# Kernel tuning notes

Measured on AMD Instinct MI355X. Metric: run time of the kernel, lower is better.

Reference implementation:

```python
import jax, jax.numpy as jnp
import numpy as np

T, D, E, F = 8192, 1024, 8, 3584


def setup_inputs() -> dict:
    key = jax.random.key(0)
    ks = jax.random.split(key, 5)
    scale_in = 1.0 / np.sqrt(D)
    scale_ff = 1.0 / np.sqrt(F)
    return {
        "x": jax.random.normal(ks[0], (T, D), dtype=jnp.float32),
        "w1": jax.random.normal(ks[1], (E, F, D), dtype=jnp.float32) * scale_in,
        "w3": jax.random.normal(ks[2], (E, F, D), dtype=jnp.float32) * scale_in,
        "w2": jax.random.normal(ks[3], (E, D, F), dtype=jnp.float32) * scale_ff,
        "router_logits": jax.random.normal(ks[4], (T, E), dtype=jnp.float32),
        "top_k": 2,
    }


def reference(x, w1, w3, w2, router_logits, top_k):
    # Routing: softmax over experts, keep top-k, renormalize (Mixtral, normalize=True)
    probs = jax.nn.softmax(router_logits, axis=-1)            # [T, E]
    top_vals, top_idx = jax.lax.top_k(probs, top_k)           # [T, k]
    top_vals = top_vals / jnp.sum(top_vals, axis=-1, keepdims=True)
    tokens = jnp.arange(x.shape[0])[:, None]
    weights = jnp.zeros_like(probs).at[tokens, top_idx].set(top_vals)  # [T, E]

    gate = jnp.einsum('td,efd->tef', x, w1)                   # [T, E, F]
    up = jnp.einsum('td,efd->tef', x, w3)                     # [T, E, F]
    h = jax.nn.silu(gate) * up                                # [T, E, F]
    out = jnp.einsum('te,tef,edf->td', weights, h, w2)        # [T, D]
    return out
```

## Files before the change

kernel.cpp:

```cpp
#include <hip/hip_runtime.h>
#include <cstdint>

#define T_TOK 8192
#define D_DIM 1024
#define E_EXP 8
#define F_DIM 3584
#define NROW  (2 * T_TOK)
#define PROWS_PAD 18432

typedef __attribute__((ext_vector_type(8))) __bf16 bf16x8;
typedef __attribute__((ext_vector_type(4))) float f32x4;

__device__ __forceinline__ void gload16(const void* g, void* l) {
    __builtin_amdgcn_global_load_lds(
        (const __attribute__((address_space(1))) void*)(g),
        (__attribute__((address_space(3))) void*)(l),
        16, 0, 0);
}

__device__ __forceinline__ int xcd_swz(int bid, int nwg) {
    const int nx = 8;
    const int q = nwg / nx, r = nwg % nx;
    const int xcd = bid % nx, lid = bid / nx;
    return (xcd < r ? xcd * (q + 1) : r * (q + 1) + (xcd - r) * q) + lid;
}

__global__ void cvt_kernel(const float* __restrict__ in, __bf16* __restrict__ out, long n) {
    long i = ((long)blockIdx.x * blockDim.x + threadIdx.x) * 8;
    if (i >= n) return;
    const float4 f0 = *(const float4*)(in + i);
    const float4 f1 = *(const float4*)(in + i + 4);
    bf16x8 o;
    o[0] = (__bf16)f0.x; o[1] = (__bf16)f0.y; o[2] = (__bf16)f0.z; o[3] = (__bf16)f0.w;
    o[4] = (__bf16)f1.x; o[5] = (__bf16)f1.y; o[6] = (__bf16)f1.z; o[7] = (__bf16)f1.w;
    *(bf16x8*)(out + i) = o;
}

__global__ void route_kernel(const float* __restrict__ rl, int* cnt,
                             int* __restrict__ eidx, float* __restrict__ ewgt) {
    int t = blockIdx.x * blockDim.x + threadIdx.x;
    if (t >= T_TOK) return;
    float l[8];
#pragma unroll
    for (int e = 0; e < 8; ++e) l[e] = rl[t * 8 + e];
    int i0 = 0; float v0 = l[0];
    int i1 = -1; float v1 = -1e30f;
#pragma unroll
    for (int e = 1; e < 8; ++e) {
        if (l[e] > v0) { v1 = v0; i1 = i0; v0 = l[e]; i0 = e; }
        else if (l[e] > v1) { v1 = l[e]; i1 = e; }
    }
    float wsec = 1.f / (1.f + __expf(v0 - v1));
    eidx[2 * t] = i0; eidx[2 * t + 1] = i1;
    ewgt[2 * t] = 1.f - wsec; ewgt[2 * t + 1] = wsec;
    atomicAdd(&cnt[i0], 1); atomicAdd(&cnt[i1], 1);
}

__global__ void scan_kernel(const int* __restrict__ cnt, int* __restrict__ pofs) {
    if (threadIdx.x == 0) {
        int a = 0;
        for (int e = 0; e < E_EXP; ++e) { pofs[e] = a; a += (cnt[e] + 255) & ~255; }
        pofs[E_EXP] = a;
    }
}

__global__ void assign_kernel(const int* __restrict__ eidx, const int* __restrict__ pofs,
                              int* cnt2, int* __restrict__ tokOf, int* __restrict__ rowOf) {
    int t = blockIdx.x * blockDim.x + threadIdx.x;
    if (t >= T_TOK) return;
#pragma unroll
    for (int s = 0; s < 2; ++s) {
        int e = eidx[2 * t + s];
        int pos = atomicAdd(&cnt2[e], 1);
        int prow = pofs[e] + pos;
        tokOf[prow] = t;
        rowOf[2 * t + s] = prow;
    }
}

__global__ void gather_kernel(const float* __restrict__ x, const int* __restrict__ tokOf,
                              __bf16* __restrict__ xg) {
    const int idx = blockIdx.x * blockDim.x + threadIdx.x;
    const int pr = idx >> 7;
    const int j = (idx & 127) * 8;
    const int tk = tokOf[pr];
    bf16x8 o = {};
    if (tk >= 0) {
        const float4 f0 = *(const float4*)(x + (long)tk * D_DIM + j);
        const float4 f1 = *(const float4*)(x + (long)tk * D_DIM + j + 4);
        o[0] = (__bf16)f0.x; o[1] = (__bf16)f0.y; o[2] = (__bf16)f0.z; o[3] = (__bf16)f0.w;
        o[4] = (__bf16)f1.x; o[5] = (__bf16)f1.y; o[6] = (__bf16)f1.z; o[7] = (__bf16)f1.w;
    }
    *(bf16x8*)(xg + (long)pr * D_DIM + j) = o;
}

__device__ __forceinline__ int chunk_row(int c) { return ((c >> 7) << 4) | ((c >> 2) & 15); }
__device__ __forceinline__ int chunk_col(int c) {
    return ((c >> 6) & 1) * 32 + (((c & 3) * 8) ^ (((c >> 5) & 1) << 4));
}

template <int NT>
__device__ __forceinline__ void moe_pipeline(
    const __bf16* const (&srcA)[2][2], const __bf16* const (&srcB)[2][2],
    __bf16 (&Ash)[2][2][8192], __bf16 (&Bsh)[2][2][8192],
    int wave, int abase, int wm, int bh, int bsel, f32x4 (&acc)[8][4])
{
    auto stA = [&](int buf, int kt, int h) {
        const long k0 = (long)kt * 64;
        gload16(srcA[h][0] + k0, &Ash[buf][h][(0 * 512 + wave * 64) * 8]);
        gload16(srcA[h][1] + k0, &Ash[buf][h][(1 * 512 + wave * 64) * 8]);
    };
    auto stB = [&](int buf, int kt, int h) {
        const long k0 = (long)kt * 64;
        gload16(srcB[h][0] + k0, &Bsh[buf][h][(0 * 512 + wave * 64) * 8]);
        gload16(srcB[h][1] + k0, &Bsh[buf][h][(1 * 512 + wave * 64) * 8]);
    };

    bf16x8 bfr[4][2];
    bf16x8 a0, a1, a2, a3;

#define LD_A(Ab, q) \
    a0 = *(const bf16x8*)((Ab) + ((2*(q)) * 2 + 0) * 512); \
    a1 = *(const bf16x8*)((Ab) + ((2*(q)) * 2 + 1) * 512); \
    a2 = *(const bf16x8*)((Ab) + ((2*(q)+1) * 2 + 0) * 512); \
    a3 = *(const bf16x8*)((Ab) + ((2*(q)+1) * 2 + 1) * 512);

#define LD_B(Bb) \
    _Pragma("unroll") for (int ni = 0; ni < 4; ++ni) { \
        bfr[ni][0] = *(const bf16x8*)((Bb) + ((bsel * 4 + ni) * 2 + 0) * 512); \
        bfr[ni][1] = *(const bf16x8*)((Bb) + ((bsel * 4 + ni) * 2 + 1) * 512); \
    }

#define MFMA_Q(q) \
    _Pragma("unroll") for (int ni = 0; ni < 4; ++ni) { \
        acc[2*(q)][ni]   = __builtin_amdgcn_mfma_f32_16x16x32_bf16(a0, bfr[ni][0], acc[2*(q)][ni], 0, 0, 0); \
        acc[2*(q)][ni]   = __builtin_amdgcn_mfma_f32_16x16x32_bf16(a1, bfr[ni][1], acc[2*(q)][ni], 0, 0, 0); \
        acc[2*(q)+1][ni] = __builtin_amdgcn_mfma_f32_16x16x32_bf16(a2, bfr[ni][0], acc[2*(q)+1][ni], 0, 0, 0); \
        acc[2*(q)+1][ni] = __builtin_amdgcn_mfma_f32_16x16x32_bf16(a3, bfr[ni][1], acc[2*(q)+1][ni], 0, 0, 0); \
    }

#define PH_OPEN() \
    __builtin_amdgcn_sched_barrier(0); \
    __builtin_amdgcn_s_barrier(); \
    asm volatile("s_waitcnt lgkmcnt(0)" ::: "memory"); \
    __builtin_amdgcn_sched_barrier(0); \
    __builtin_amdgcn_s_setprio(1);

#define PH_CLOSE() \
    __builtin_amdgcn_s_setprio(0); \
    __builtin_amdgcn_sched_barrier(0); \
    __builtin_amdgcn_s_barrier(); \
    __builtin_amdgcn_sched_barrier(0);

#define PH_CLOSE_G(lastf) \
    __builtin_amdgcn_s_setprio(0); \
    __builtin_amdgcn_sched_barrier(0); \
    if (lastf) { asm volatile("s_waitcnt vmcnt(0)" ::: "memory"); } \
    else       { asm volatile("s_waitcnt vmcnt(4)" ::: "memory"); } \
    __builtin_amdgcn_s_barrier(); \
    __builtin_amdgcn_sched_barrier(0);

    stA(0, 0, 0); stA(0, 0, 1); stB(0, 0, 0); stB(0, 0, 1);
    stB(1, 1, 0); stB(1, 1, 1);
    asm volatile("s_waitcnt vmcnt(4)" ::: "memory");
    __builtin_amdgcn_s_barrier();

    const __bf16* AbE = &Ash[0][wm][abase];
    const __bf16* BbE = &Bsh[0][bh][abase];
    const __bf16* AbO = &Ash[1][wm][abase];
    const __bf16* BbO = &Bsh[1][bh][abase];

    for (int it = 0; it < NT / 2; ++it) {
        const int kv = 2 * it + 1;
        const bool last = (it == NT / 2 - 1);
        LD_A(AbE, 0) LD_B(BbE)
        stA(1, kv, 0);
        PH_OPEN() MFMA_Q(0) PH_CLOSE()
        LD_A(AbE, 1)
        stA(1, kv, 1);
        PH_OPEN() MFMA_Q(1) PH_CLOSE()
        LD_A(AbE, 2)
        if (!last) stB(0, kv + 1, 0);
        PH_OPEN() MFMA_Q(2) PH_CLOSE()
        LD_A(AbE, 3)
        if (!last) stB(0, kv + 1, 1);
        PH_OPEN() MFMA_Q(3) PH_CLOSE_G(last)
        LD_A(AbO, 0) LD_B(BbO)
        if (!last) stA(0, kv + 1, 0);
        PH_OPEN() MFMA_Q(0) PH_CLOSE()
        LD_A(AbO, 1)
        if (!last) stA(0, kv + 1, 1);
        PH_OPEN() MFMA_Q(1) PH_CLOSE()
        LD_A(AbO, 2)
        if (!last) stB(1, kv + 2, 0);
        PH_OPEN() MFMA_Q(2) PH_CLOSE()
        LD_A(AbO, 3)
        if (!last) stB(1, kv + 2, 1);
        PH_OPEN() MFMA_Q(3) PH_CLOSE_G(last)
    }
#undef LD_A
#undef LD_B
#undef MFMA_Q
#undef PH_OPEN
#undef PH_CLOSE
#undef PH_CLOSE_G
}

__global__ __launch_bounds__(512, 1)
void gemm1_kernel(const __bf16* __restrict__ xg,
                  const __bf16* __restrict__ w1b,
                  const __bf16* __restrict__ w3b,
                  const int* __restrict__ pofs,
                  __bf16* __restrict__ h) {
    const int NX = F_DIM / 128, NY = T_TOK / 256;
    const int nwg = NX * NY * E_EXP;
    int w = xcd_swz(blockIdx.x + NX * (blockIdx.y + NY * blockIdx.z), nwg);
    const int nt = w % NX; w /= NX;
    const int mt = w % NY; w /= NY;
    const int e = w;
    const int row0 = pofs[e];
    const int prows = pofs[e + 1] - row0;
    if (mt * 256 >= prows) return;

    __shared__ __align__(16) __bf16 Ash[2][2][8192];
    __shared__ __align__(16) __bf16 Bsh[2][2][8192];

    const int tid = threadIdx.x;
    const int wave = tid >> 6, lane = tid & 63;
    const int wm = wave >> 2, wn = wave & 3;
    const int fr = lane & 15, fg = lane >> 4;

    const __bf16* srcA[2][2];
    const __bf16* srcB[2][2];
#pragma unroll
    for (int half = 0; half < 2; ++half)
#pragma unroll
        for (int j = 0; j < 2; ++j) {
            const int c = tid + j * 512;
            srcA[half][j] = xg + (long)(row0 + mt * 256 + half * 128 + chunk_row(c)) * D_DIM + chunk_col(c);
            const int rb = half * 128 + chunk_row(c);
            const int blk = rb >> 4;
            const int f = nt * 128 + (blk >> 1) * 16 + (rb & 15);
            srcB[half][j] = ((blk & 1) ? w3b : w1b) + ((long)e * F_DIM + f) * D_DIM + chunk_col(c);
        }

    const int abase = fr * 32 + ((fg * 8) ^ ((fr & 8) << 1));
    f32x4 acc[8][4] = {};

    moe_pipeline<16>(srcA, srcB, Ash, Bsh, wave, abase, wm, wn >> 1, wn & 1, acc);

#pragma unroll
    for (int mi = 0; mi < 8; ++mi) {
#pragma unroll
        for (int reg = 0; reg < 4; ++reg) {
            const int lm = mt * 256 + wm * 128 + mi * 16 + fg * 4 + reg;
            const long hrow = (long)(row0 + lm) * F_DIM;
#pragma unroll
            for (int b = 0; b < 2; ++b) {
                const float g = acc[mi][2 * b][reg];
                const float u = acc[mi][2 * b + 1][reg];
                const float s = g / (1.f + __expf(-g));
                h[hrow + nt * 128 + (wn * 2 + b) * 16 + fr] = (__bf16)(s * u);
            }
        }
    }
}

__global__ __launch_bounds__(512, 1)
void gemm2_kernel(const __bf16* __restrict__ hb,
                  const __bf16* __restrict__ w2b,
                  const int* __restrict__ pofs,
                  __bf16* __restrict__ o2p) {
    const int NX = D_DIM / 256, NY = T_TOK / 256;
    const int nwg = NX * NY * E_EXP * 2;
    int w = xcd_swz(blockIdx.x + NX * (blockIdx.y + NY * blockIdx.z), nwg);
    const int nt = w % NX; w /= NX;
    const int mt = w % NY; w /= NY;
    const int e = w >> 1, ks = w & 1;
    const int row0 = pofs[e];
    const int prows = pofs[e + 1] - row0;
    if (mt * 256 >= prows) return;

    __shared__ __align__(16) __bf16 Ash[2][2][8192];
    __shared__ __align__(16) __bf16 Bsh[2][2][8192];

    const int tid = threadIdx.x;
    const int wave = tid >> 6, lane = tid & 63;
    const int wm = wave >> 2, wn = wave & 3;
    const int fr = lane & 15, fg = lane >> 4;
    const int kofs = ks * (F_DIM / 2);

    const __bf16* srcA[2][2];
    const __bf16* srcB[2][2];
#pragma unroll
    for (int half = 0; half < 2; ++half)
#pragma unroll
        for (int j = 0; j < 2; ++j) {
            const int c = tid + j * 512;
            srcA[half][j] = hb + (long)(row0 + mt * 256 + half * 128 + chunk_row(c)) * F_DIM + kofs + chunk_col(c);
            const int rb = half * 128 + chunk_row(c);
            srcB[half][j] = w2b + ((long)e * D_DIM + nt * 256 + rb) * F_DIM + kofs + chunk_col(c);
        }

    const int abase = fr * 32 + ((fg * 8) ^ ((fr & 8) << 1));
    f32x4 acc[8][4] = {};

    moe_pipeline<28>(srcA, srcB, Ash, Bsh, wave, abase, wm, wn >> 1, wn & 1, acc);

    __bf16* ps = o2p + (long)ks * PROWS_PAD * D_DIM;
#pragma unroll
    for (int mi = 0; mi < 8; ++mi) {
#pragma unroll
        for (int reg = 0; reg < 4; ++reg) {
            const int lm = mt * 256 + wm * 128 + mi * 16 + fg * 4 + reg;
            const long obase = (long)(row0 + lm) * D_DIM + nt * 256 + wn * 64 + fr;
#pragma unroll
            for (int ni = 0; ni < 4; ++ni)
                ps[obase + ni * 16] = (__bf16)acc[mi][ni][reg];
        }
    }
}

__global__ void combine_kernel(const __bf16* __restrict__ o2p, const int* __restrict__ rowOf,
                               const float* __restrict__ ewgt, float* __restrict__ out) {
    const int idx = blockIdx.x * blockDim.x + threadIdx.x;
    const int t = idx >> 7;
    const int j = (idx & 127) * 8;
    const long r0 = rowOf[2 * t], r1 = rowOf[2 * t + 1];
    const float w0 = ewgt[2 * t], w1 = ewgt[2 * t + 1];
    float r[8] = {0, 0, 0, 0, 0, 0, 0, 0};
#pragma unroll
    for (int s = 0; s < 2; ++s) {
        const bf16x8 a = *(const bf16x8*)(o2p + ((long)s * PROWS_PAD + r0) * D_DIM + j);
        const bf16x8 b = *(const bf16x8*)(o2p + ((long)s * PROWS_PAD + r1) * D_DIM + j);
#pragma unroll
        for (int q = 0; q < 8; ++q) r[q] += w0 * (float)a[q] + w1 * (float)b[q];
    }
    float4* ob = (float4*)(out + (long)t * D_DIM + j);
    ob[0] = make_float4(r[0], r[1], r[2], r[3]);
    ob[1] = make_float4(r[4], r[5], r[6], r[7]);
}

extern "C" void kernel_launch(void* const* d_in, const int* in_sizes, int n_in,
                              void* d_out, int out_size, void* d_ws, size_t ws_size,
                              hipStream_t stream) {
    const float* x  = (const float*)d_in[0];
    const float* w1 = (const float*)d_in[1];
    const float* w3 = (const float*)d_in[2];
    const float* w2 = (const float*)d_in[3];
    const float* rl = (const float*)d_in[4];
    float* out = (float*)d_out;

    char* ws = (char*)d_ws;
    size_t off = 0;
    auto alloc = [&](size_t bytes) {
        void* p = ws + off;
        off += (bytes + 255) & ~(size_t)255;
        return p;
    };
    __bf16* xg   = (__bf16*)alloc((size_t)PROWS_PAD * D_DIM * 2);
    __bf16* w1b  = (__bf16*)alloc((size_t)E_EXP * F_DIM * D_DIM * 2);
    __bf16* w3b  = (__bf16*)alloc((size_t)E_EXP * F_DIM * D_DIM * 2);
    __bf16* hbuf = (__bf16*)alloc((size_t)PROWS_PAD * F_DIM * 2);
    int*   tokOf = (int*)alloc(PROWS_PAD * 4);
    int*   rowOf = (int*)alloc(NROW * 4);
    int*   eidx  = (int*)alloc(NROW * 4);
    float* ewgt  = (float*)alloc(NROW * 4);
    int*   cnt1  = (int*)alloc(64);
    int*   cnt2  = (int*)alloc(64);
    int*   pofs  = (int*)alloc(64);
    __bf16* w2b = (__bf16*)ws;
    __bf16* o2p = (__bf16*)(ws + (size_t)E_EXP * D_DIM * F_DIM * 2);

    hipMemsetAsync(cnt1, 0, 64, stream);
    hipMemsetAsync(cnt2, 0, 64, stream);
    hipMemsetAsync(tokOf, 0xFF, PROWS_PAD * 4, stream);

    route_kernel<<<T_TOK / 256, 256, 0, stream>>>(rl, cnt1, eidx, ewgt);
    scan_kernel<<<1, 64, 0, stream>>>(cnt1, pofs);
    assign_kernel<<<T_TOK / 256, 256, 0, stream>>>(eidx, pofs, cnt2, tokOf, rowOf);
    gather_kernel<<<PROWS_PAD * 128 / 256, 256, 0, stream>>>(x, tokOf, xg);

    {
        const long n = (long)E_EXP * F_DIM * D_DIM;
        const int blks = (int)(n / 8 / 256);
        cvt_kernel<<<blks, 256, 0, stream>>>(w1, w1b, n);
        cvt_kernel<<<blks, 256, 0, stream>>>(w3, w3b, n);
    }

    dim3 g1(F_DIM / 128, T_TOK / 256, E_EXP);
    gemm1_kernel<<<g1, 512, 0, stream>>>(xg, w1b, w3b, pofs, hbuf);

    {
        const long n = (long)E_EXP * D_DIM * F_DIM;
        cvt_kernel<<<(int)(n / 8 / 256), 256, 0, stream>>>(w2, w2b, n);
    }

    dim3 g2(D_DIM / 256, T_TOK / 256, E_EXP * 2);
    gemm2_kernel<<<g2, 512, 0, stream>>>(hbuf, w2b, pofs, o2p);

    combine_kernel<<<T_TOK * (D_DIM / 8) / 256, 256, 0, stream>>>(o2p, rowOf, ewgt, out);
}
```

Before: 701.5 us.

## Schedule GEMM workgroups from a compact tile list with banded L2-friendly ordering

Adds a tiles kernel that lists every (expert, 256-row) tile actually in use. Both grouped GEMMs now launch a 1D grid over this compact list instead of a dense (N, M, E) grid where most blocks exit early. Tiles are grouped into bands of four, and each XCD gets a contiguous range of work so neighbouring blocks share A rows and weight columns in cache. The cost is one extra serial kernel launch and a new block-to-tile mapping that replaces the old XCD swizzle.

```diff
diff --git a/kernel.cpp b/kernel.cpp
--- a/kernel.cpp
+++ b/kernel.cpp
@@ -7,6 +7,8 @@
 #define F_DIM 3584
 #define NROW  (2 * T_TOK)
 #define PROWS_PAD 18432
+#define MAXTILES 72
+#define MAXBANDS 18
 
 typedef __attribute__((ext_vector_type(8))) __bf16 bf16x8;
 typedef __attribute__((ext_vector_type(4))) float f32x4;
@@ -16,13 +18,6 @@
         (const __attribute__((address_space(1))) void*)(g),
         (__attribute__((address_space(3))) void*)(l),
         16, 0, 0);
-}
-
-__device__ __forceinline__ int xcd_swz(int bid, int nwg) {
-    const int nx = 8;
-    const int q = nwg / nx, r = nwg % nx;
-    const int xcd = bid % nx, lid = bid / nx;
-    return (xcd < r ? xcd * (q + 1) : r * (q + 1) + (xcd - r) * q) + lid;
 }
 
 __global__ void cvt_kernel(const float* __restrict__ in, __bf16* __restrict__ out, long n) {
@@ -61,6 +56,18 @@
         int a = 0;
         for (int e = 0; e < E_EXP; ++e) { pofs[e] = a; a += (cnt[e] + 255) & ~255; }
         pofs[E_EXP] = a;
+    }
+}
+
+__global__ void tiles_kernel(const int* __restrict__ pofs, int* __restrict__ tile_e,
+                             int* __restrict__ tile_r0, int* __restrict__ meta) {
+    if (threadIdx.x == 0) {
+        int n = 0;
+        for (int e = 0; e < E_EXP; ++e)
+            for (int r = pofs[e]; r < pofs[e + 1]; r += 256) {
+                tile_e[n] = e; tile_r0[n] = r; ++n;
+            }
+        meta[0] = n;
     }
 }
 
@@ -210,17 +217,22 @@
 void gemm1_kernel(const __bf16* __restrict__ xg,
                   const __bf16* __restrict__ w1b,
                   const __bf16* __restrict__ w3b,
-                  const int* __restrict__ pofs,
+                  const int* __restrict__ tile_e,
+                  const int* __restrict__ tile_r0,
+                  const int* __restrict__ meta,
                   __bf16* __restrict__ h) {
-    const int NX = F_DIM / 128, NY = T_TOK / 256;
-    const int nwg = NX * NY * E_EXP;
-    int w = xcd_swz(blockIdx.x + NX * (blockIdx.y + NY * blockIdx.z), nwg);
-    const int nt = w % NX; w /= NX;
-    const int mt = w % NY; w /= NY;
-    const int e = w;
-    const int row0 = pofs[e];
-    const int prows = pofs[e + 1] - row0;
-    if (mt * 256 >= prows) return;
+    const int count = meta[0];
+    const int bands = (count + 3) >> 2;
+    const int live = bands * 112;
+    const int bid = blockIdx.x;
+    if (bid >= live) return;
+    const int w = (bid & 7) * (live >> 3) + (bid >> 3);
+    const int q28 = w / 28, r = w % 28;
+    const int tile = (q28 >> 2) * 4 + r / 7;
+    const int nt = (q28 & 3) * 7 + r % 7;
+    if (tile >= count) return;
+    const int e = tile_e[tile];
+    const int row0 = tile_r0[tile];
 
     __shared__ __align__(16) __bf16 Ash[2][2][8192];
     __shared__ __align__(16) __bf16 Bsh[2][2][8192];
@@ -237,7 +249,7 @@
 #pragma unroll
         for (int j = 0; j < 2; ++j) {
             const int c = tid + j * 512;
-            srcA[half][j] = xg + (long)(row0 + mt * 256 + half * 128 + chunk_row(c)) * D_DIM + chunk_col(c);
+            srcA[half][j] = xg + (long)(row0 + half * 128 + chunk_row(c)) * D_DIM + chunk_col(c);
             const int rb = half * 128 + chunk_row(c);
             const int blk = rb >> 4;
             const int f = nt * 128 + (blk >> 1) * 16 + (rb & 15);
@@ -253,7 +265,7 @@
     for (int mi = 0; mi < 8; ++mi) {
 #pragma unroll
         for (int reg = 0; reg < 4; ++reg) {
-            const int lm = mt * 256 + wm * 128 + mi * 16 + fg * 4 + reg;
+            const int lm = wm * 128 + mi * 16 + fg * 4 + reg;
             const long hrow = (long)(row0 + lm) * F_DIM;
 #pragma unroll
             for (int b = 0; b < 2; ++b) {
@@ -269,17 +281,22 @@
 __global__ __launch_bounds__(512, 1)
 void gemm2_kernel(const __bf16* __restrict__ hb,
                   const __bf16* __restrict__ w2b,
-                  const int* __restrict__ pofs,
+                  const int* __restrict__ tile_e,
+                  const int* __restrict__ tile_r0,
+                  const int* __restrict__ meta,
                   __bf16* __restrict__ o2p) {
-    const int NX = D_DIM / 256, NY = T_TOK / 256;
-    const int nwg = NX * NY * E_EXP * 2;
-    int w = xcd_swz(blockIdx.x + NX * (blockIdx.y + NY * blockIdx.z), nwg);
-    const int nt = w % NX; w /= NX;
-    const int mt = w % NY; w /= NY;
-    const int e = w >> 1, ks = w & 1;
-    const int row0 = pofs[e];
-    const int prows = pofs[e + 1] - row0;
-    if (mt * 256 >= prows) return;
+    const int count = meta[0];
+    const int bands = (count + 3) >> 2;
+    const int live = bands * 32;
+    const int bid = blockIdx.x;
+    if (bid >= live) return;
+    const int w = (bid & 7) * (live >> 3) + (bid >> 3);
+    const int band = w >> 5, s = w & 31;
+    const int tile = band * 4 + (s >> 3);
+    const int nt = s & 3, ks = (s >> 2) & 1;
+    if (tile >= count) return;
+    const int e = tile_e[tile];
+    const int row0 = tile_r0[tile];
 
     __shared__ __align__(16) __bf16 Ash[2][2][8192];
     __shared__ __align__(16) __bf16 Bsh[2][2][8192];
@@ -297,7 +314,7 @@
 #pragma unroll
         for (int j = 0; j < 2; ++j) {
             const int c = tid + j * 512;
-            srcA[half][j] = hb + (long)(row0 + mt * 256 + half * 128 + chunk_row(c)) * F_DIM + kofs + chunk_col(c);
+            srcA[half][j] = hb + (long)(row0 + half * 128 + chunk_row(c)) * F_DIM + kofs + chunk_col(c);
             const int rb = half * 128 + chunk_row(c);
             srcB[half][j] = w2b + ((long)e * D_DIM + nt * 256 + rb) * F_DIM + kofs + chunk_col(c);
         }
@@ -312,7 +329,7 @@
     for (int mi = 0; mi < 8; ++mi) {
 #pragma unroll
         for (int reg = 0; reg < 4; ++reg) {
-            const int lm = mt * 256 + wm * 128 + mi * 16 + fg * 4 + reg;
+            const int lm = wm * 128 + mi * 16 + fg * 4 + reg;
             const long obase = (long)(row0 + lm) * D_DIM + nt * 256 + wn * 64 + fr;
 #pragma unroll
             for (int ni = 0; ni < 4; ++ni)
@@ -369,6 +386,9 @@
     int*   cnt1  = (int*)alloc(64);
     int*   cnt2  = (int*)alloc(64);
     int*   pofs  = (int*)alloc(64);
+    int*   tileE = (int*)alloc(MAXTILES * 4 + 64);
+    int*   tileR = (int*)alloc(MAXTILES * 4 + 64);
+    int*   meta  = (int*)alloc(64);
     __bf16* w2b = (__bf16*)ws;
     __bf16* o2p = (__bf16*)(ws + (size_t)E_EXP * D_DIM * F_DIM * 2);
 
@@ -378,6 +398,7 @@
 
     route_kernel<<<T_TOK / 256, 256, 0, stream>>>(rl, cnt1, eidx, ewgt);
     scan_kernel<<<1, 64, 0, stream>>>(cnt1, pofs);
+    tiles_kernel<<<1, 64, 0, stream>>>(pofs, tileE, tileR, meta);
     assign_kernel<<<T_TOK / 256, 256, 0, stream>>>(eidx, pofs, cnt2, tokOf, rowOf);
     gather_kernel<<<PROWS_PAD * 128 / 256, 256, 0, stream>>>(x, tokOf, xg);
 
@@ -388,16 +409,14 @@
         cvt_kernel<<<blks, 256, 0, stream>>>(w3, w3b, n);
     }
 
-    dim3 g1(F_DIM / 128, T_TOK / 256, E_EXP);
-    gemm1_kernel<<<g1, 512, 0, stream>>>(xg, w1b, w3b, pofs, hbuf);
+    gemm1_kernel<<<MAXBANDS * 112, 512, 0, stream>>>(xg, w1b, w3b, tileE, tileR, meta, hbuf);
 
     {
         const long n = (long)E_EXP * D_DIM * F_DIM;
         cvt_kernel<<<(int)(n / 8 / 256), 256, 0, stream>>>(w2, w2b, n);
     }
 
-    dim3 g2(D_DIM / 256, T_TOK / 256, E_EXP * 2);
-    gemm2_kernel<<<g2, 512, 0, stream>>>(hbuf, w2b, pofs, o2p);
+    gemm2_kernel<<<MAXBANDS * 32, 512, 0, stream>>>(hbuf, w2b, tileE, tileR, meta, o2p);
 
     combine_kernel<<<T_TOK * (D_DIM / 8) / 256, 256, 0, stream>>>(o2p, rowOf, ewgt, out);
 }
```

Result: no change. 695.5 us (-0.8%).
